# Performance work log

Hardware: AMD Instinct MI355X
Metric: run time of the kernel (lower is better)

## Reference

```python
import jax, jax.numpy as jnp
import numpy as np

NUM_HEADS = 4

def _pos_encoding(seq_len, d, dtype):
    # standard sinusoidal positional encoding [seq_len, d]
    pos = jnp.arange(seq_len, dtype=jnp.float32)[:, None]
    i = jnp.arange(0, d, 2, dtype=jnp.float32)
    div = jnp.exp(-jnp.log(10000.0) * i / d)
    ang = pos * div
    pe = jnp.zeros((seq_len, d), jnp.float32)
    pe = pe.at[:, 0::2].set(jnp.sin(ang)).at[:, 1::2].set(jnp.cos(ang))
    return pe.astype(dtype)

def _layer_norm(x, g, b, eps=1e-5):
    m = jnp.mean(x, axis=-1, keepdims=True)
    v = jnp.mean(jnp.square(x - m), axis=-1, keepdims=True)
    return (x - m) / jnp.sqrt(v + eps) * g + b

def setup_inputs() -> dict:
    key = jax.random.key(0)
    ks = jax.random.split(key, 10)
    B, S, H, W, N = 8, 512, 768, 8, 4096
    s = 0.02
    token_reps = jax.random.normal(ks[0], (B, S, H), jnp.float32)
    starts = jax.random.randint(ks[1], (B, N), 0, S - W)
    widths = jax.random.randint(ks[2], (B, N), 1, W + 1)
    span_ids = jnp.stack([starts, starts + widths], axis=-1)  # end > start, end <= S
    span_masks = jax.random.randint(ks[3], (B, N), 0, 2)
    return dict(
        token_reps=token_reps,
        dummy_query=jax.random.normal(ks[4], (H,), jnp.float32) * s,
        in_proj_w=jax.random.normal(ks[5], (3 * H, H), jnp.float32) * s,
        in_proj_b=jnp.zeros((3 * H,), jnp.float32),
        out_w=jax.random.normal(ks[6], (H, H), jnp.float32) * s,
        out_b=jnp.zeros((H,), jnp.float32),
        ln_g=jnp.ones((H,), jnp.float32),
        ln_b=jnp.zeros((H,), jnp.float32),
        ffn_w1=jax.random.normal(ks[7], (H, 4 * H), jnp.float32) * s,
        ffn_b1=jnp.zeros((4 * H,), jnp.float32),
        ffn_w2=jax.random.normal(ks[8], (4 * H, H), jnp.float32) * s,
        ffn_b2=jnp.zeros((H,), jnp.float32),
        span_ids=span_ids,
        span_masks=span_masks,
    )

def reference(token_reps, dummy_query, in_proj_w, in_proj_b, out_w, out_b,
              ln_g, ln_b, ffn_w1, ffn_b1, ffn_w2, ffn_b2, span_ids, span_masks):
    B, S, H = token_reps.shape
    N = span_ids.shape[1]
    NH = NUM_HEADS
    DH = H // NH
    # sequence positional encoding (dropout is identity in eval mode)
    x = token_reps + _pos_encoding(S, H, token_reps.dtype)[None]
    Wq, Wk, Wv = jnp.split(in_proj_w, 3, axis=0)
    bq, bk, bv = jnp.split(in_proj_b, 3)
    # single shared dummy query -> per-head query [NH, DH]
    q = (dummy_query @ Wq.T + bq).reshape(NH, DH)
    k = (x @ Wk.T + bk).reshape(B, S, NH, DH)
    v = (x @ Wv.T + bv).reshape(B, S, NH, DH)
    # scores are identical across spans since the query is shared: [B, NH, S]
    scores = jnp.einsum('hd,bshd->bhs', q, k) / jnp.sqrt(jnp.asarray(DH, x.dtype))
    pos = jnp.arange(S)
    # per-span key validity: start <= pos < end, and span not masked out  [B, N, S]
    valid = (pos[None, None, :] >= span_ids[..., 0:1]) & \
            (pos[None, None, :] < span_ids[..., 1:2]) & \
            (span_masks[..., None] != 0)
    logits = jnp.where(valid[:, :, None, :], scores[:, None, :, :], -1e9)  # [B,N,NH,S]
    w = jax.nn.softmax(logits, axis=-1)
    attn = jnp.einsum('bnhs,bshd->bnhd', w, v).reshape(B, N, H)
    attn = attn @ out_w.T + out_b
    h1 = _layer_norm(attn + dummy_query, ln_g, ln_b)
    ffn = jax.nn.relu(h1 @ ffn_w1 + ffn_b1) @ ffn_w2 + ffn_b2
    out = _layer_norm(ffn + h1, ln_g, ln_b)
    # masked spans produce exact zeros, matching the original loop
    return out * (span_masks[..., None] != 0).astype(out.dtype)
```

## Files before the change

### kernel.cpp

```cpp
#include <hip/hip_runtime.h>
#include <hip/hip_bf16.h>

#define Bb 8
#define Ss 512
#define Hh 768
#define NHh 4
#define Nn 4096
#define ROWS (Bb * Nn)
#define SCB 128
#define CHROWS 16384

typedef _Float16 f16x8 __attribute__((ext_vector_type(8)));
typedef _Float16 f16x4 __attribute__((ext_vector_type(4)));
typedef _Float16 f16x2 __attribute__((ext_vector_type(2)));
typedef float f32x4 __attribute__((ext_vector_type(4)));

#define DEVINL __device__ __forceinline__

DEVINL void gld_lds16(const void* g, void* l) {
  __builtin_amdgcn_global_load_lds(
      (const __attribute__((address_space(1))) void*)g,
      (__attribute__((address_space(3))) void*)l, 16, 0, 0);
}

template <int V>
DEVINL void wait_vmcnt() {
  if constexpr (V == 0) asm volatile("s_waitcnt vmcnt(0)" ::: "memory");
  else if constexpr (V == 3) asm volatile("s_waitcnt vmcnt(3)" ::: "memory");
  else if constexpr (V == 4) asm volatile("s_waitcnt vmcnt(4)" ::: "memory");
  else if constexpr (V == 6) asm volatile("s_waitcnt vmcnt(6)" ::: "memory");
  else if constexpr (V == 8) asm volatile("s_waitcnt vmcnt(8)" ::: "memory");
}

DEVINL float block_sum256(float v, float* red) {
#pragma unroll
  for (int o = 32; o; o >>= 1) v += __shfl_xor(v, o, 64);
  const int wid = threadIdx.x >> 6, lane = threadIdx.x & 63;
  if (lane == 0) red[wid] = v;
  __syncthreads();
  float r = red[0] + red[1] + red[2] + red[3];
  __syncthreads();
  return r;
}

__global__ __launch_bounds__(256) void x_kernel(const float* __restrict__ tok,
                                                _Float16* __restrict__ x) {
  int idx = blockIdx.x * 256 + threadIdx.x;
  int t = idx % 384;
  int bs = idx / 384;
  int s = bs & (Ss - 1);
  float div = expf(-(float)t * 0.02398526138535465f);
  float ang = (float)s * div;
  float sv = sinf(ang), cv = cosf(ang);
  const float2 tv = ((const float2*)tok)[(size_t)bs * 384 + t];
  f16x2 o;
  o[0] = (_Float16)(tv.x + sv);
  o[1] = (_Float16)(tv.y + cv);
  *(f16x2*)&x[(size_t)bs * Hh + 2 * t] = o;
}

__global__ __launch_bounds__(256) void q_kernel(const float* __restrict__ dq,
                                                const float* __restrict__ ipw,
                                                const float* __restrict__ ipb,
                                                float* __restrict__ qout) {
  __shared__ float red[4];
  int o = blockIdx.x;
  const float* wr = ipw + (size_t)o * Hh;
  float s = 0.f;
#pragma unroll
  for (int e = 0; e < 3; e++) {
    int j = threadIdx.x + 256 * e;
    s += dq[j] * wr[j];
  }
  s = block_sum256(s, red);
  if (threadIdx.x == 0) qout[o] = s + ipb[o];
}

__global__ __launch_bounds__(256) void c_kernel(const float* __restrict__ q,
                                                const float* __restrict__ ipw,
                                                const float* __restrict__ ipb,
                                                float* __restrict__ cout,
                                                float* __restrict__ sbias) {
  __shared__ float red[4];
  int bid = blockIdx.x;
  int t = threadIdx.x;
  if (bid < 3072) {
    int h = bid / Hh;
    int j = bid - h * Hh;
    float s = 0.f;
    if (t < 192) s = q[h * 192 + t] * ipw[(size_t)(Hh + h * 192 + t) * Hh + j];
    s = block_sum256(s, red);
    if (t == 0) cout[bid] = s;
  } else {
    int h = bid - 3072;
    float s = 0.f;
    if (t < 192) s = q[h * 192 + t] * ipb[Hh + h * 192 + t];
    s = block_sum256(s, red);
    if (t == 0) sbias[h] = s;
  }
}

__global__ __launch_bounds__(256) void score_kernel(
    const _Float16* __restrict__ x, const float* __restrict__ c,
    const float* __restrict__ sbias, float* __restrict__ scores) {
  int bs = blockIdx.x;
  int wid = threadIdx.x >> 6, lane = threadIdx.x & 63;
  const _Float16* xr = x + (size_t)bs * Hh;
  const float* ch = c + wid * Hh;
  float s = 0.f;
#pragma unroll
  for (int e = 0; e < 12; e++) {
    int j = e * 64 + lane;
    s += (float)xr[j] * ch[j];
  }
#pragma unroll
  for (int o = 32; o; o >>= 1) s += __shfl_xor(s, o, 64);
  if (lane == 0) {
    int b = bs >> 9, pos = bs & (Ss - 1);
    scores[((size_t)(b * NHh + wid)) * Ss + pos] =
        (s + sbias[wid]) * 0.07216878364870322f;
  }
}

__global__ __launch_bounds__(256) void cvt_kernel(const float* __restrict__ in,
                                                  _Float16* __restrict__ out) {
  int i = blockIdx.x * 256 + threadIdx.x;
  float4 f = ((const float4*)in)[i];
  f16x4 o;
  o[0] = (_Float16)f.x;
  o[1] = (_Float16)f.y;
  o[2] = (_Float16)f.z;
  o[3] = (_Float16)f.w;
  ((f16x4*)out)[i] = o;
}

__global__ __launch_bounds__(256) void trcvt_kernel(const float* __restrict__ in,
                                                    _Float16* __restrict__ out,
                                                    int R, int C) {
  __shared__ float tile[32][33];
  int c0 = blockIdx.x * 32, r0 = blockIdx.y * 32;
  int tx = threadIdx.x & 31, ty0 = threadIdx.x >> 5;
#pragma unroll
  for (int ty = ty0; ty < 32; ty += 8)
    tile[ty][tx] = in[(size_t)(r0 + ty) * C + c0 + tx];
  __syncthreads();
#pragma unroll
  for (int ty = ty0; ty < 32; ty += 8)
    out[(size_t)(c0 + ty) * R + r0 + tx] = (_Float16)tile[tx][ty];
}

__global__ __launch_bounds__(256) void scan1_kernel(const int* __restrict__ mask,
                                                    int* __restrict__ bsum) {
  int r = blockIdx.x * 256 + threadIdx.x;
  unsigned long long b = __ballot(mask[r] != 0);
  __shared__ int wsum[4];
  int lane = threadIdx.x & 63, wid = threadIdx.x >> 6;
  if (lane == 0) wsum[wid] = __popcll(b);
  __syncthreads();
  if (threadIdx.x == 0)
    bsum[blockIdx.x] = wsum[0] + wsum[1] + wsum[2] + wsum[3];
}
__global__ __launch_bounds__(64) void scan2_kernel(const int* __restrict__ bsum,
                                                   int* __restrict__ boff,
                                                   int* __restrict__ cnt) {
  if (threadIdx.x == 0) {
    int acc = 0;
    for (int i = 0; i < SCB; i++) {
      boff[i] = acc;
      acc += bsum[i];
    }
    *cnt = acc;
  }
}
__global__ __launch_bounds__(256) void cidx_kernel(const int* __restrict__ mask,
                                                   const int* __restrict__ boff,
                                                   int* __restrict__ cidx) {
  int r = blockIdx.x * 256 + threadIdx.x;
  int m = mask[r] != 0;
  unsigned long long b = __ballot(m);
  __shared__ int wsum[4];
  int lane = threadIdx.x & 63, wid = threadIdx.x >> 6;
  if (lane == 0) wsum[wid] = __popcll(b);
  __syncthreads();
  int pre = 0;
#pragma unroll
  for (int i = 0; i < 3; i++)
    if (i < wid) pre += wsum[i];
  pre += __popcll(b & ((1ULL << lane) - 1));
  if (m) cidx[r] = boff[blockIdx.x] + pre;
}

#define ITER_RESTAGE(b, knext)              \
  do {                                      \
    wait_vmcnt<2 * LPS>();                  \
    __builtin_amdgcn_s_barrier();           \
    COMPUTE(b);                             \
    __builtin_amdgcn_s_barrier();           \
    STAGE(b, (knext));                      \
  } while (0)
#define PIPE_MAIN()                         \
  const int nt = KK >> 5;                   \
  STAGE(0, 0);                              \
  STAGE(1, 32);                             \
  STAGE(2, 64);                             \
  int t = 0;                                \
  for (; t <= nt - 6; t += 3) {             \
    ITER_RESTAGE(0, (t + 3) * 32);          \
    ITER_RESTAGE(1, (t + 4) * 32);          \
    ITER_RESTAGE(2, (t + 5) * 32);          \
  }                                         \
  wait_vmcnt<2 * LPS>();                    \
  __builtin_amdgcn_s_barrier();             \
  COMPUTE(0);                               \
  wait_vmcnt<LPS>();                        \
  __builtin_amdgcn_s_barrier();             \
  COMPUTE(1);                               \
  wait_vmcnt<0>();                          \
  __builtin_amdgcn_s_barrier();             \
  COMPUTE(2);

template <int RELU, int BN>
__global__ __launch_bounds__(256, 2) void gemm_nt(
    const _Float16* __restrict__ A, const _Float16* __restrict__ W,
    const float* __restrict__ bias, _Float16* __restrict__ C, int N, int K,
    int nn, const int* __restrict__ mcount) {
  const int bid = (int)blockIdx.x;
  const int mi = (bid >> 3) / nn;
  const int nt_ = (bid >> 3) - mi * nn;
  const long m0 = (long)(mi * 8 + (bid & 7)) * 128;
  const long n0 = (long)nt_ * BN;
  if (mcount && m0 >= (long)*mcount) return;
  __shared__ __align__(16) _Float16 As[3][128 * 32];
  __shared__ __align__(16) _Float16 Bs[3][BN * 32];
  const int tid = threadIdx.x;
  const int wid = tid >> 6;
  const int lane = tid & 63;
  constexpr int LPS = (BN == 128) ? 4 : 3;
  const int KK = K;

  const int c0 = wid * 64 + lane;
  const int c1 = c0 + 256;
  const int sw0 = ((c0 & 3) ^ ((c0 >> 3) & 3)) * 8;
  const int sw1 = ((c1 & 3) ^ ((c1 >> 3) & 3)) * 8;
  const _Float16* gA0 = A + (m0 + (c0 >> 2)) * K + sw0;
  const _Float16* gA1 = A + (m0 + (c1 >> 2)) * K + sw1;
  const _Float16* gB0 = W + (n0 + (c0 >> 2)) * K + sw0;
  const _Float16* gB1 = W + (n0 + (c1 >> 2)) * K + sw1;

  const int wr = (wid >> 1) * 64;
  const int wc = (wid & 1) * (BN / 2);
  constexpr int NF = BN / 32;
  const int fr = lane & 15;
  const int fkb = lane >> 4;

  f32x4 acc[4][NF];
#pragma unroll
  for (int mi2 = 0; mi2 < 4; mi2++)
#pragma unroll
    for (int ni = 0; ni < NF; ni++) acc[mi2][ni] = (f32x4){0.f, 0.f, 0.f, 0.f};

#define STAGE(buf, k0)                                                  \
  do {                                                                  \
    gld_lds16(gA0 + (k0), &As[buf][wid * 512]);                         \
    gld_lds16(gA1 + (k0), &As[buf][2048 + wid * 512]);                  \
    gld_lds16(gB0 + (k0), &Bs[buf][wid * 512]);                         \
    if constexpr (BN == 128) gld_lds16(gB1 + (k0), &Bs[buf][2048 + wid * 512]); \
  } while (0)

#define COMPUTE(buf)                                                          \
  do {                                                                        \
    f16x8 af[4], bf[NF];                                                      \
    _Pragma("unroll") for (int i = 0; i < 4; i++) {                           \
      int r_ = wr + i * 16 + fr;                                              \
      af[i] = *(const f16x8*)&As[buf][r_ * 32 + ((fkb ^ ((r_ >> 1) & 3)) * 8)]; \
    }                                                                         \
    _Pragma("unroll") for (int i = 0; i < NF; i++) {                          \
      int r_ = wc + i * 16 + fr;                                              \
      bf[i] = *(const f16x8*)&Bs[buf][r_ * 32 + ((fkb ^ ((r_ >> 1) & 3)) * 8)]; \
    }                                                                         \
    __builtin_amdgcn_s_setprio(1);                                            \
    _Pragma("unroll") for (int mi2 = 0; mi2 < 4; mi2++)                       \
        _Pragma("unroll") for (int ni = 0; ni < NF; ni++)                     \
            acc[mi2][ni] = __builtin_amdgcn_mfma_f32_16x16x32_f16(            \
                af[mi2], bf[ni], acc[mi2][ni], 0, 0, 0);                      \
    __builtin_amdgcn_s_setprio(0);                                            \
  } while (0)

  PIPE_MAIN()
#undef STAGE
#undef COMPUTE

  const int crow = (lane >> 4) * 4;
  const int ccol = lane & 15;
  float bv[NF];
#pragma unroll
  for (int ni = 0; ni < NF; ni++)
    bv[ni] = bias ? bias[n0 + wc + ni * 16 + ccol] : 0.f;
#pragma unroll
  for (int mi2 = 0; mi2 < 4; mi2++)
#pragma unroll
    for (int ni = 0; ni < NF; ni++)
#pragma unroll
      for (int i = 0; i < 4; i++) {
        float v = acc[mi2][ni][i] + bv[ni];
        if (RELU) v = fmaxf(v, 0.f);
        C[(m0 + wr + mi2 * 16 + crow + i) * (long)N + (n0 + wc + ni * 16 + ccol)] =
            (_Float16)v;
      }
}

template <int RELU, int SPLIT>
__global__ __launch_bounds__(512, 4) void gemm8_nt(
    const _Float16* __restrict__ A, const _Float16* __restrict__ W,
    const float* __restrict__ bias, _Float16* __restrict__ C0,
    _Float16* __restrict__ C1, int N, int K, int nn, int mbase,
    const int* __restrict__ mcount) {
  int bid = (int)blockIdx.x;
  int half = 0;
  if constexpr (SPLIT == 2) {
    const int hg = (int)gridDim.x >> 1;
    half = bid >= hg;
    bid -= half * hg;
  }
  const int mi = (bid >> 3) / nn;
  const int nt_ = (bid >> 3) - mi * nn;
  const long m0 = (long)(mi * 8 + (bid & 7)) * 256;
  const long n0 = (long)nt_ * 128;
  if (mcount && (long)mbase + m0 >= (long)*mcount) return;
  const int KK = K / SPLIT;
  const int koff = half * KK;
  _Float16* C = half ? C1 : C0;
  const float* biasp = (SPLIT == 2 && half == 1) ? nullptr : bias;

  __shared__ __align__(16) _Float16 As[3][256 * 32];
  __shared__ __align__(16) _Float16 Bs[3][128 * 32];
  const int tid = threadIdx.x;
  const int w = tid >> 6;
  const int lane = tid & 63;
  constexpr int LPS = 3;

  const int rA0 = w * 16 + (lane >> 2);
  const int rA1 = rA0 + 128;
  const int cb = lane & 3;
  const int swA0 = (cb ^ ((rA0 >> 1) & 3)) * 8;
  const int swA1 = (cb ^ ((rA1 >> 1) & 3)) * 8;
  const _Float16* gA0 = A + (m0 + rA0) * K + koff + swA0;
  const _Float16* gA1 = A + (m0 + rA1) * K + koff + swA1;
  const _Float16* gB0 = W + (n0 + rA0) * K + koff + swA0;

  const int wr = (w >> 1) * 64;
  const int wc = (w & 1) * 64;
  const int fr = lane & 15;
  const int fkb = lane >> 4;

  f32x4 acc[4][4];
#pragma unroll
  for (int mi2 = 0; mi2 < 4; mi2++)
#pragma unroll
    for (int ni = 0; ni < 4; ni++) acc[mi2][ni] = (f32x4){0.f, 0.f, 0.f, 0.f};

#define STAGE(buf, k0)                                   \
  do {                                                   \
    gld_lds16(gA0 + (k0), &As[buf][w * 512]);            \
    gld_lds16(gA1 + (k0), &As[buf][(w + 8) * 512]);      \
    gld_lds16(gB0 + (k0), &Bs[buf][w * 512]);            \
  } while (0)

#define COMPUTE(buf)                                                          \
  do {                                                                        \
    f16x8 af[4], bf[4];                                                       \
    _Pragma("unroll") for (int i = 0; i < 4; i++) {                           \
      int r_ = wr + i * 16 + fr;                                              \
      af[i] = *(const f16x8*)&As[buf][r_ * 32 + ((fkb ^ ((r_ >> 1) & 3)) * 8)]; \
    }                                                                         \
    _Pragma("unroll") for (int i = 0; i < 4; i++) {                           \
      int r_ = wc + i * 16 + fr;                                              \
      bf[i] = *(const f16x8*)&Bs[buf][r_ * 32 + ((fkb ^ ((r_ >> 1) & 3)) * 8)]; \
    }                                                                         \
    __builtin_amdgcn_s_setprio(1);                                            \
    _Pragma("unroll") for (int mi2 = 0; mi2 < 4; mi2++)                       \
        _Pragma("unroll") for (int ni = 0; ni < 4; ni++)                      \
            acc[mi2][ni] = __builtin_amdgcn_mfma_f32_16x16x32_f16(            \
                af[mi2], bf[ni], acc[mi2][ni], 0, 0, 0);                      \
    __builtin_amdgcn_s_setprio(0);                                            \
  } while (0)

  PIPE_MAIN()
#undef STAGE
#undef COMPUTE

  const int crow = (lane >> 4) * 4;
  const int ccol = lane & 15;
  float bv[4];
#pragma unroll
  for (int ni = 0; ni < 4; ni++)
    bv[ni] = biasp ? biasp[n0 + wc + ni * 16 + ccol] : 0.f;
#pragma unroll
  for (int mi2 = 0; mi2 < 4; mi2++)
#pragma unroll
    for (int ni = 0; ni < 4; ni++)
#pragma unroll
      for (int i = 0; i < 4; i++) {
        float v = acc[mi2][ni][i] + bv[ni];
        if (RELU) v = fmaxf(v, 0.f);
        C[(m0 + wr + mi2 * 16 + crow + i) * (long)N + (n0 + wc + ni * 16 + ccol)] =
            (_Float16)v;
      }
}

__global__ __launch_bounds__(192) void pool_kernel(
    const _Float16* __restrict__ v, const float* __restrict__ scores,
    const int* __restrict__ span_ids, const int* __restrict__ span_masks,
    _Float16* __restrict__ attn, const int* __restrict__ cidx) {
  int r = blockIdx.x;
  if (span_masks[r] == 0) return;
  int slot = cidx[r];
  int i = threadIdx.x;
  int h = i / 48;
  int d0 = i * 4;
  int b = r >> 12;
  int st = span_ids[2 * r], en = span_ids[2 * r + 1];
  int wdt = en - st;
  const float* sc = scores + ((size_t)(b * NHh + h)) * Ss + st;
  float w[8];
  float mx = -1e30f;
#pragma unroll
  for (int j = 0; j < 8; j++) {
    float t = (j < wdt) ? sc[j] : -1e30f;
    w[j] = t;
    mx = fmaxf(mx, t);
  }
  float sum = 0.f;
#pragma unroll
  for (int j = 0; j < 8; j++) {
    float e = (j < wdt) ? expf(w[j] - mx) : 0.f;
    w[j] = e;
    sum += e;
  }
  float inv = 1.f / sum;
  float a0 = 0.f, a1 = 0.f, a2 = 0.f, a3 = 0.f;
#pragma unroll
  for (int j = 0; j < 8; j++) {
    if (j < wdt) {
      f16x4 vv = *(const f16x4*)(v + ((size_t)(b * Ss + st + j)) * Hh + d0);
      float wj = w[j] * inv;
      a0 += wj * (float)vv[0];
      a1 += wj * (float)vv[1];
      a2 += wj * (float)vv[2];
      a3 += wj * (float)vv[3];
    }
  }
  f16x4 o;
  o[0] = (_Float16)a0;
  o[1] = (_Float16)a1;
  o[2] = (_Float16)a2;
  o[3] = (_Float16)a3;
  *(f16x4*)&attn[(size_t)slot * Hh + d0] = o;
}

__global__ __launch_bounds__(256) void ln0_kernel(
    _Float16* __restrict__ XA, const _Float16* __restrict__ XB,
    const float* __restrict__ AddV, const float* __restrict__ g,
    const float* __restrict__ bta, const int* __restrict__ mcount) {
  __shared__ float red[4];
  int r = blockIdx.x;
  if (r >= *mcount) return;
  int t = threadIdx.x;
  float xv[3];
#pragma unroll
  for (int e = 0; e < 3; e++) {
    int d = t + 256 * e;
    xv[e] = (float)XA[(size_t)r * Hh + d] + (float)XB[(size_t)r * Hh + d] +
            AddV[d];
  }
  float s = xv[0] + xv[1] + xv[2];
  s = block_sum256(s, red);
  float mean = s * (1.f / 768.f);
  float vs = 0.f;
#pragma unroll
  for (int e = 0; e < 3; e++) {
    float d = xv[e] - mean;
    vs += d * d;
  }
  vs = block_sum256(vs, red);
  float inv = rsqrtf(vs * (1.f / 768.f) + 1e-5f);
#pragma unroll
  for (int e = 0; e < 3; e++) {
    int d = t + 256 * e;
    XA[(size_t)r * Hh + d] = (_Float16)((xv[e] - mean) * inv * g[d] + bta[d]);
  }
}

__global__ __launch_bounds__(256) void ln1_kernel(
    const _Float16* __restrict__ F2a, const _Float16* __restrict__ F2b,
    const _Float16* __restrict__ h1c, const int* __restrict__ cidx,
    const float* __restrict__ g, const float* __restrict__ bta,
    const int* __restrict__ mask, float* __restrict__ out) {
  __shared__ float red[4];
  int r = blockIdx.x;
  int t = threadIdx.x;
  float* orow = out + (size_t)r * Hh;
  if (mask[r] == 0) {
#pragma unroll
    for (int e = 0; e < 3; e++) orow[t + 256 * e] = 0.f;
    return;
  }
  int c = cidx[r];
  float xv[3];
#pragma unroll
  for (int e = 0; e < 3; e++) {
    int d = t + 256 * e;
    xv[e] = (float)F2a[(size_t)c * Hh + d] + (float)F2b[(size_t)c * Hh + d] +
            (float)h1c[(size_t)c * Hh + d];
  }
  float s = xv[0] + xv[1] + xv[2];
  s = block_sum256(s, red);
  float mean = s * (1.f / 768.f);
  float vs = 0.f;
#pragma unroll
  for (int e = 0; e < 3; e++) {
    float d = xv[e] - mean;
    vs += d * d;
  }
  vs = block_sum256(vs, red);
  float inv = rsqrtf(vs * (1.f / 768.f) + 1e-5f);
#pragma unroll
  for (int e = 0; e < 3; e++) {
    int d = t + 256 * e;
    orow[d] = (xv[e] - mean) * inv * g[d] + bta[d];
  }
}

extern "C" void kernel_launch(void* const* d_in, const int* in_sizes, int n_in,
                              void* d_out, int out_size, void* d_ws,
                              size_t ws_size, hipStream_t stream) {
  (void)out_size;
  if (n_in != 14) return;
  if (in_sizes[0] != 3145728 || in_sizes[2] != 1769472 ||
      in_sizes[3] != 2304 || in_sizes[4] != 589824 ||
      in_sizes[8] != 2359296 || in_sizes[9] != 3072 ||
      in_sizes[12] != 65536 || in_sizes[13] != 32768)
    return;

  const float* tok   = (const float*)d_in[0];
  const float* dq    = (const float*)d_in[1];
  const float* ipw   = (const float*)d_in[2];
  const float* ipb   = (const float*)d_in[3];
  const float* outw  = (const float*)d_in[4];
  const float* outb  = (const float*)d_in[5];
  const float* lng   = (const float*)d_in[6];
  const float* lnb   = (const float*)d_in[7];
  const float* w1    = (const float*)d_in[8];
  const float* b1    = (const float*)d_in[9];
  const float* w2    = (const float*)d_in[10];
  const float* b2    = (const float*)d_in[11];
  const int* spid    = (const int*)d_in[12];
  const int* spmask  = (const int*)d_in[13];

  char* ws = (char*)d_ws;
  size_t off = 0;
  auto alloc = [&](size_t bytes) {
    size_t r = off;
    off = (off + bytes + 255) & ~(size_t)255;
    return r;
  };
  _Float16* X16  = (_Float16*)(ws + alloc((size_t)Bb * Ss * Hh * 2));
  float* SC      = (float*)(ws + alloc((size_t)Bb * NHh * Ss * 4));
  float* Q       = (float*)(ws + alloc(768 * 4));
  float* Cc      = (float*)(ws + alloc(3072 * 4));
  float* SB      = (float*)(ws + alloc(4 * 4));
  _Float16* WV16 = (_Float16*)(ws + alloc((size_t)768 * 768 * 2));
  _Float16* OW16 = (_Float16*)(ws + alloc((size_t)768 * 768 * 2));
  _Float16* WT1  = (_Float16*)(ws + alloc((size_t)3072 * 768 * 2));
  _Float16* WT2  = (_Float16*)(ws + alloc((size_t)768 * 3072 * 2));
  _Float16* ATTN = (_Float16*)(ws + alloc((size_t)ROWS * Hh * 2));
  _Float16* PROJ = (_Float16*)(ws + alloc((size_t)ROWS * Hh * 2));
  _Float16* PB   = (_Float16*)(ws + alloc((size_t)ROWS * Hh * 2));
  _Float16* F1   = (_Float16*)(ws + alloc((size_t)CHROWS * 3072 * 2));
  if (ws_size < off) return;
  _Float16* F2A = ATTN;
  _Float16* F2B = PB;

  int* CIDX = (int*)X16;
  int* BSUM = (int*)X16 + ROWS;
  int* BOFF = (int*)X16 + ROWS + SCB;
  int* CNT  = (int*)X16 + ROWS + 2 * SCB;

  _Float16* V16 = (_Float16*)d_out;

  cvt_kernel<<<576, 256, 0, stream>>>(ipw + (size_t)1536 * 768, WV16);
  cvt_kernel<<<576, 256, 0, stream>>>(outw, OW16);
  trcvt_kernel<<<dim3(96, 24), 256, 0, stream>>>(w1, WT1, 768, 3072);
  trcvt_kernel<<<dim3(24, 96), 256, 0, stream>>>(w2, WT2, 3072, 768);

  x_kernel<<<(Bb * Ss * 384) / 256, 256, 0, stream>>>(tok, X16);
  q_kernel<<<768, 256, 0, stream>>>(dq, ipw, ipb, Q);
  c_kernel<<<3076, 256, 0, stream>>>(Q, ipw, ipb, Cc, SB);
  score_kernel<<<Bb * Ss, 256, 0, stream>>>(X16, Cc, SB, SC);
  gemm_nt<0, 64><<<384, 256, 0, stream>>>(X16, WV16, ipb + 1536, V16,
                                          768, 768, 12, nullptr);
  scan1_kernel<<<SCB, 256, 0, stream>>>(spmask, BSUM);
  scan2_kernel<<<1, 64, 0, stream>>>(BSUM, BOFF, CNT);
  cidx_kernel<<<SCB, 256, 0, stream>>>(spmask, BOFF, CIDX);
  pool_kernel<<<ROWS, 192, 0, stream>>>(V16, SC, spid, spmask, ATTN, CIDX);
  gemm8_nt<0, 2><<<1536, 512, 0, stream>>>(ATTN, OW16, outb, PROJ, PB,
                                           768, 768, 6, 0, CNT);
  ln0_kernel<<<ROWS, 256, 0, stream>>>(PROJ, PB, dq, lng, lnb, CNT);
  for (int ch = 0; ch < 2; ch++) {
    const int mb = ch * CHROWS;
    gemm8_nt<1, 1><<<1536, 512, 0, stream>>>(
        PROJ + (size_t)mb * Hh, WT1, b1, F1, nullptr, 3072, 768, 24, mb, CNT);
    gemm8_nt<0, 2><<<768, 512, 0, stream>>>(
        F1, WT2, b2, F2A + (size_t)mb * Hh, F2B + (size_t)mb * Hh,
        768, 3072, 6, mb, CNT);
  }
  ln1_kernel<<<ROWS, 256, 0, stream>>>(F2A, F2B, PROJ, CIDX, lng, lnb, spmask,
                                       (float*)d_out);
}
```

Baseline: 414.9 us.

## Drop split-K in projection and FFN2 GEMMs and run FFN2 unchunked

Removes the two-way split-K path from the 256x128 GEMM kernel. The output projection and the second FFN GEMM now each write one result buffer, so the LayerNorm kernels read a single GEMM output instead of summing two partial buffers. F1 is allocated for all rows so FFN2 can run as one launch after both FFN1 chunks. This saves the extra partial-sum writes and reads and one buffer, but halves the number of blocks per GEMM launch. Since compacted rows cut the active tile count, the GEMMs may leave compute units idle.

```diff
diff --git a/kernel.cpp b/kernel.cpp
--- a/kernel.cpp
+++ b/kernel.cpp
@@ -199,7 +199,7 @@
     STAGE(b, (knext));                      \
   } while (0)
 #define PIPE_MAIN()                         \
-  const int nt = KK >> 5;                   \
+  const int nt = K >> 5;                    \
   STAGE(0, 0);                              \
   STAGE(1, 32);                             \
   STAGE(2, 64);                             \
@@ -236,7 +236,6 @@
   const int wid = tid >> 6;
   const int lane = tid & 63;
   constexpr int LPS = (BN == 128) ? 4 : 3;
-  const int KK = K;
 
   const int c0 = wid * 64 + lane;
   const int c1 = c0 + 256;
@@ -309,29 +308,17 @@
       }
 }
 
-template <int RELU, int SPLIT>
+template <int RELU>
 __global__ __launch_bounds__(512, 4) void gemm8_nt(
     const _Float16* __restrict__ A, const _Float16* __restrict__ W,
-    const float* __restrict__ bias, _Float16* __restrict__ C0,
-    _Float16* __restrict__ C1, int N, int K, int nn, int mbase,
-    const int* __restrict__ mcount) {
-  int bid = (int)blockIdx.x;
-  int half = 0;
-  if constexpr (SPLIT == 2) {
-    const int hg = (int)gridDim.x >> 1;
-    half = bid >= hg;
-    bid -= half * hg;
-  }
+    const float* __restrict__ bias, _Float16* __restrict__ C, int N, int K,
+    int nn, int mbase, const int* __restrict__ mcount) {
+  const int bid = (int)blockIdx.x;
   const int mi = (bid >> 3) / nn;
   const int nt_ = (bid >> 3) - mi * nn;
   const long m0 = (long)(mi * 8 + (bid & 7)) * 256;
   const long n0 = (long)nt_ * 128;
   if (mcount && (long)mbase + m0 >= (long)*mcount) return;
-  const int KK = K / SPLIT;
-  const int koff = half * KK;
-  _Float16* C = half ? C1 : C0;
-  const float* biasp = (SPLIT == 2 && half == 1) ? nullptr : bias;
-
   __shared__ __align__(16) _Float16 As[3][256 * 32];
   __shared__ __align__(16) _Float16 Bs[3][128 * 32];
   const int tid = threadIdx.x;
@@ -344,9 +331,9 @@
   const int cb = lane & 3;
   const int swA0 = (cb ^ ((rA0 >> 1) & 3)) * 8;
   const int swA1 = (cb ^ ((rA1 >> 1) & 3)) * 8;
-  const _Float16* gA0 = A + (m0 + rA0) * K + koff + swA0;
-  const _Float16* gA1 = A + (m0 + rA1) * K + koff + swA1;
-  const _Float16* gB0 = W + (n0 + rA0) * K + koff + swA0;
+  const _Float16* gA0 = A + (m0 + rA0) * K + swA0;
+  const _Float16* gA1 = A + (m0 + rA1) * K + swA1;
+  const _Float16* gB0 = W + (n0 + rA0) * K + swA0;
 
   const int wr = (w >> 1) * 64;
   const int wc = (w & 1) * 64;
@@ -394,7 +381,7 @@
   float bv[4];
 #pragma unroll
   for (int ni = 0; ni < 4; ni++)
-    bv[ni] = biasp ? biasp[n0 + wc + ni * 16 + ccol] : 0.f;
+    bv[ni] = bias ? bias[n0 + wc + ni * 16 + ccol] : 0.f;
 #pragma unroll
   for (int mi2 = 0; mi2 < 4; mi2++)
 #pragma unroll
@@ -459,9 +446,9 @@
 }
 
 __global__ __launch_bounds__(256) void ln0_kernel(
-    _Float16* __restrict__ XA, const _Float16* __restrict__ XB,
-    const float* __restrict__ AddV, const float* __restrict__ g,
-    const float* __restrict__ bta, const int* __restrict__ mcount) {
+    _Float16* __restrict__ X, const float* __restrict__ AddV,
+    const float* __restrict__ g, const float* __restrict__ bta,
+    const int* __restrict__ mcount) {
   __shared__ float red[4];
   int r = blockIdx.x;
   if (r >= *mcount) return;
@@ -470,8 +457,7 @@
 #pragma unroll
   for (int e = 0; e < 3; e++) {
     int d = t + 256 * e;
-    xv[e] = (float)XA[(size_t)r * Hh + d] + (float)XB[(size_t)r * Hh + d] +
-            AddV[d];
+    xv[e] = (float)X[(size_t)r * Hh + d] + AddV[d];
   }
   float s = xv[0] + xv[1] + xv[2];
   s = block_sum256(s, red);
@@ -487,15 +473,15 @@
 #pragma unroll
   for (int e = 0; e < 3; e++) {
     int d = t + 256 * e;
-    XA[(size_t)r * Hh + d] = (_Float16)((xv[e] - mean) * inv * g[d] + bta[d]);
+    X[(size_t)r * Hh + d] = (_Float16)((xv[e] - mean) * inv * g[d] + bta[d]);
   }
 }
 
 __global__ __launch_bounds__(256) void ln1_kernel(
-    const _Float16* __restrict__ F2a, const _Float16* __restrict__ F2b,
-    const _Float16* __restrict__ h1c, const int* __restrict__ cidx,
-    const float* __restrict__ g, const float* __restrict__ bta,
-    const int* __restrict__ mask, float* __restrict__ out) {
+    const _Float16* __restrict__ F2c, const _Float16* __restrict__ h1c,
+    const int* __restrict__ cidx, const float* __restrict__ g,
+    const float* __restrict__ bta, const int* __restrict__ mask,
+    float* __restrict__ out) {
   __shared__ float red[4];
   int r = blockIdx.x;
   int t = threadIdx.x;
@@ -510,8 +496,7 @@
 #pragma unroll
   for (int e = 0; e < 3; e++) {
     int d = t + 256 * e;
-    xv[e] = (float)F2a[(size_t)c * Hh + d] + (float)F2b[(size_t)c * Hh + d] +
-            (float)h1c[(size_t)c * Hh + d];
+    xv[e] = (float)F2c[(size_t)c * Hh + d] + (float)h1c[(size_t)c * Hh + d];
   }
   float s = xv[0] + xv[1] + xv[2];
   s = block_sum256(s, red);
@@ -575,11 +560,9 @@
   _Float16* WT2  = (_Float16*)(ws + alloc((size_t)768 * 3072 * 2));
   _Float16* ATTN = (_Float16*)(ws + alloc((size_t)ROWS * Hh * 2));
   _Float16* PROJ = (_Float16*)(ws + alloc((size_t)ROWS * Hh * 2));
-  _Float16* PB   = (_Float16*)(ws + alloc((size_t)ROWS * Hh * 2));
-  _Float16* F1   = (_Float16*)(ws + alloc((size_t)CHROWS * 3072 * 2));
+  _Float16* F1   = (_Float16*)(ws + alloc((size_t)ROWS * 3072 * 2));
   if (ws_size < off) return;
-  _Float16* F2A = ATTN;
-  _Float16* F2B = PB;
+  _Float16* F2 = ATTN;
 
   int* CIDX = (int*)X16;
   int* BSUM = (int*)X16 + ROWS;
@@ -603,17 +586,17 @@
   scan2_kernel<<<1, 64, 0, stream>>>(BSUM, BOFF, CNT);
   cidx_kernel<<<SCB, 256, 0, stream>>>(spmask, BOFF, CIDX);
   pool_kernel<<<ROWS, 192, 0, stream>>>(V16, SC, spid, spmask, ATTN, CIDX);
-  gemm8_nt<0, 2><<<1536, 512, 0, stream>>>(ATTN, OW16, outb, PROJ, PB,
-                                           768, 768, 6, 0, CNT);
-  ln0_kernel<<<ROWS, 256, 0, stream>>>(PROJ, PB, dq, lng, lnb, CNT);
+  gemm8_nt<0><<<768, 512, 0, stream>>>(ATTN, OW16, outb, PROJ,
+                                       768, 768, 6, 0, CNT);
+  ln0_kernel<<<ROWS, 256, 0, stream>>>(PROJ, dq, lng, lnb, CNT);
   for (int ch = 0; ch < 2; ch++) {
     const int mb = ch * CHROWS;
-    gemm8_nt<1, 1><<<1536, 512, 0, stream>>>(
-        PROJ + (size_t)mb * Hh, WT1, b1, F1, nullptr, 3072, 768, 24, mb, CNT);
-    gemm8_nt<0, 2><<<768, 512, 0, stream>>>(
-        F1, WT2, b2, F2A + (size_t)mb * Hh, F2B + (size_t)mb * Hh,
-        768, 3072, 6, mb, CNT);
-  }
-  ln1_kernel<<<ROWS, 256, 0, stream>>>(F2A, F2B, PROJ, CIDX, lng, lnb, spmask,
+    gemm8_nt<1><<<1536, 512, 0, stream>>>(
+        PROJ + (size_t)mb * Hh, WT1, b1, F1 + (size_t)mb * 3072,
+        3072, 768, 24, mb, CNT);
+  }
+  gemm8_nt<0><<<768, 512, 0, stream>>>(F1, WT2, b2, F2,
+                                       768, 3072, 6, 0, CNT);
+  ln1_kernel<<<ROWS, 256, 0, stream>>>(F2, PROJ, CIDX, lng, lnb, spmask,
                                        (float*)d_out);
 }
```

Result: faster. 376.9 us (-9.2%).
